# Kernel optimization log

Measured on AMD Instinct MI355X. Metric: run time of the kernel, lower is better.

The kernel has to match this reference:

```python
import jax, jax.numpy as jnp
import numpy as np

D, FF, R, B, S, H, HD = 1024, 4096, 16, 8, 512, 16, 64
EPS = 1e-5


def _lora(x, w, b, la, lb):
    # base linear (w is [out,in] torch-style) + low-rank LoRA add
    return x @ w.T + b + (x @ la) @ lb


def _ln(x, w, b):
    mu = jnp.mean(x, axis=-1, keepdims=True)
    var = jnp.mean((x - mu) ** 2, axis=-1, keepdims=True)
    return (x - mu) * jax.lax.rsqrt(var + EPS) * w + b


def setup_inputs() -> dict:
    key = jax.random.key(0)
    ks = jax.random.split(key, 32)
    i = iter(range(32))
    nrm = lambda shape, scale=0.02: jax.random.normal(ks[next(i)], shape, jnp.float32) * scale
    inp = {
        'x': jax.random.normal(ks[next(i)], (B, S, D), jnp.float32),
        'attention_mask': jnp.zeros((B, 1, 1, S), jnp.float32),
        'w_q': nrm((D, D)), 'b_q': nrm((D,)), 'la_q': nrm((D, R)), 'lb_q': nrm((R, D)),
        'w_k': nrm((D, D)), 'b_k': nrm((D,)), 'la_k': nrm((D, R)), 'lb_k': nrm((R, D)),
        'w_v': nrm((D, D)), 'b_v': nrm((D,)), 'la_v': nrm((D, R)), 'lb_v': nrm((R, D)),
        'w_o': nrm((D, D)), 'b_o': nrm((D,)), 'la_o': nrm((D, R)), 'lb_o': nrm((R, D)),
        'nw1': jnp.ones((D,), jnp.float32), 'nb1': jnp.zeros((D,), jnp.float32),
        'w_up': nrm((FF, D)), 'b_up': nrm((FF,)), 'la_up': nrm((D, R)), 'lb_up': nrm((R, FF)),
        'w_down': nrm((D, FF)), 'b_down': nrm((D,)), 'la_down': nrm((FF, R)), 'lb_down': nrm((R, D)),
        'nw2': jnp.ones((D,), jnp.float32), 'nb2': jnp.zeros((D,), jnp.float32),
        'num_heads': H, 'head_dim': HD,
    }
    return inp


def reference(x, attention_mask, w_q, b_q, la_q, lb_q, w_k, b_k, la_k, lb_k,
              w_v, b_v, la_v, lb_v, w_o, b_o, la_o, lb_o, nw1, nb1,
              w_up, b_up, la_up, lb_up, w_down, b_down, la_down, lb_down,
              nw2, nb2, num_heads, head_dim):
    bsz, q_len, d = x.shape
    to_heads = lambda t: t.reshape(bsz, q_len, num_heads, head_dim).transpose(0, 2, 1, 3)
    q = to_heads(_lora(x, w_q, b_q, la_q, lb_q))  # [B,H,S,HD]
    k = to_heads(_lora(x, w_k, b_k, la_k, lb_k))
    v = to_heads(_lora(x, w_v, b_v, la_v, lb_v))
    s = jnp.einsum('bhqd,bhkd->bhqk', q, k) / np.sqrt(head_dim) + attention_mask
    a = jax.nn.softmax(s, axis=-1)
    o = jnp.einsum('bhqk,bhkd->bhqd', a, v).transpose(0, 2, 1, 3).reshape(bsz, q_len, d)
    o_final = _lora(o, w_o, b_o, la_o, lb_o) + x
    x_medium = _ln(o_final, nw1, nb1)
    up = _lora(x_medium, w_up, b_up, la_up, lb_up)
    fn = jax.nn.gelu(up, approximate=False)  # torch F.gelu default = exact erf
    down = _lora(fn, w_down, b_down, la_down, lb_down) + x_medium
    return _ln(down, nw2, nb2)
```

## Files before the change

### kernel.cpp

```cpp
#include <hip/hip_runtime.h>
#include <math.h>

typedef unsigned short u16;
typedef __attribute__((ext_vector_type(8))) short short8;
typedef __attribute__((ext_vector_type(4))) float floatx4;

#define DEV __device__ __forceinline__

DEV u16 f2bs(float f){ union{float f; unsigned u;} v; v.f=f; unsigned r = v.u + 0x7fffu + ((v.u>>16)&1u); return (u16)(r>>16); }
DEV float bs2f(u16 u){ union{float f; unsigned u;} v; v.u = ((unsigned)u)<<16; return v.f; }

DEV float gelu_f(float x){
  float u2 = 2.f * x * (0.7978845608028654f + 0.03567740813636141f*x*x);
  float e = __expf(u2);
  float th = 1.f - 2.f/(e + 1.f);
  return 0.5f*x*(1.f + th);
}

#define GLL16(G,L) __builtin_amdgcn_global_load_lds((__attribute__((address_space(1))) const void*)(G), (__attribute__((address_space(3))) void*)(L), 16, 0, 0)

enum { EP_BF16=0, EP_F32RES=3, EP_GELU=4 };

DEV void swizzle_bid(int orig, int gx, int gy, int& bx, int& by){
  const int nwg = gx*gy;
  const int q = nwg >> 3, r = nwg & 7;
  const int xcd = orig & 7, idx = orig >> 3;
  const int logical = (xcd < r) ? xcd*(q+1) + idx : r*(q+1) + (xcd-r)*q + idx;
  const int G = 8;
  const int per = G*gx;
  const int gid = logical / per;
  const int rem = logical - gid*per;
  const int by0 = gid*G;
  const int rows = min(G, gy - by0);
  by = by0 + rem % rows;
  bx = rem / rows;
}

template<int MODE,bool LORA,bool SWZ>
__global__ __launch_bounds__(512) void gemm8(
    const u16* __restrict__ A, int lda,
    const u16* __restrict__ B, int ldb,
    int K,
    u16* __restrict__ obf, float* __restrict__ of32, int ldc,
    const float* __restrict__ bias,
    const u16* __restrict__ tA, int tlda,
    const u16* __restrict__ lbB,
    const float* __restrict__ resid)
{
  __shared__ u16 sm8[65536];
  const int tid = threadIdx.x;
  const int lane = tid & 63, wave = tid >> 6;
  const int wr = wave >> 2, wc = wave & 3;
  const int row16 = lane & 15, kgrp = lane >> 4;
  int bx = blockIdx.x, by = blockIdx.y;
  if constexpr (SWZ)
    swizzle_bid(blockIdx.y*gridDim.x + blockIdx.x, gridDim.x, gridDim.y, bx, by);
  const int bm0 = by*256, bn0 = bx*256;
  const u16* Ab = A + (long)bm0*lda;
  const u16* Bb = B + (long)bn0*ldb;
  const int tsel = (LORA && tlda==192) ? ((bn0>>10)*64) : 0;
  const int srow = lane >> 3;
  const int gcol = ((lane&7) ^ srow) * 8;
  const int nKT = K >> 6;
  const int nIT = nKT + (LORA ? 1 : 0);

  auto stage_half = [&](int kt, int h, int buf){
    const int isB = h & 1, hi = h >> 1;
    const u16* src; long ld;
    if (!LORA || kt < nKT){
      if (isB){ src = Bb + kt*64; ld = ldb; } else { src = Ab + kt*64; ld = lda; }
    } else {
      if (isB){ src = lbB + (long)bn0*64; ld = 64; }
      else    { src = tA + (long)bm0*tlda + tsel; ld = tlda; }
    }
    char* base = (char*)sm8 + buf*65536 + isB*32768 + hi*16384;
    #pragma unroll
    for (int rr=0; rr<2; ++rr){
      int g = wave + rr*8;
      GLL16(src + (long)(hi*128 + g*8 + srow)*ld + gcol, base + g*1024);
    }
  };
  auto ldA = [&](int buf, int mh, int i, int ks)->short8{
    int r_ = mh*128 + wr*64 + i*16 + row16;
    return *(const short8*)((const char*)sm8 + buf*65536 + r_*128 + (((ks*4+kgrp) ^ (r_&7))<<4));
  };
  auto ldB = [&](int buf, int nh, int j, int ks)->short8{
    int r_ = nh*128 + wc*32 + j*16 + row16;
    return *(const short8*)((const char*)sm8 + buf*65536 + 32768 + r_*128 + (((ks*4+kgrp) ^ (r_&7))<<4));
  };

  floatx4 acc[8][4];
  #pragma unroll
  for (int i=0;i<8;i++)
    #pragma unroll
    for (int j=0;j<4;j++)
      acc[i][j] = (floatx4){0.f,0.f,0.f,0.f};

  stage_half(0,0,0); stage_half(0,1,0); stage_half(0,2,0); stage_half(0,3,0);
  if (nIT>1){ stage_half(1,0,1); stage_half(1,1,1); }

#define MM8(mh,nh) \
  { _Pragma("unroll") \
    for (int i=0;i<4;i++) \
      _Pragma("unroll") \
      for (int j=0;j<2;j++) \
        _Pragma("unroll") \
        for (int ks=0;ks<2;ks++) \
          acc[(mh)*4+i][(nh)*2+j] = __builtin_amdgcn_mfma_f32_16x16x32_bf16(afr[i][ks], bfr[j][ks], acc[(mh)*4+i][(nh)*2+j], 0, 0, 0); }

  int buf = 0;
  for (int t=0; t<nIT; ++t, buf^=1){
    const bool n1 = (t+1 < nIT), n2 = (t+2 < nIT);
    short8 afr[4][2], bfr[2][2];
    if (n1) asm volatile("s_waitcnt vmcnt(4)" ::: "memory");
    else    asm volatile("s_waitcnt vmcnt(0)" ::: "memory");
    __builtin_amdgcn_s_barrier();
    #pragma unroll
    for (int i=0;i<4;i++){ afr[i][0]=ldA(buf,0,i,0); afr[i][1]=ldA(buf,0,i,1); }
    #pragma unroll
    for (int j=0;j<2;j++){ bfr[j][0]=ldB(buf,0,j,0); bfr[j][1]=ldB(buf,0,j,1); }
    if (n1){ stage_half(t+1,2,buf^1); stage_half(t+1,3,buf^1); }
    asm volatile("s_waitcnt lgkmcnt(0)" ::: "memory");
    __builtin_amdgcn_sched_barrier(0);
    __builtin_amdgcn_s_setprio(1);
    MM8(0,0);
    __builtin_amdgcn_s_setprio(0);
    __builtin_amdgcn_s_barrier();
    #pragma unroll
    for (int j=0;j<2;j++){ bfr[j][0]=ldB(buf,1,j,0); bfr[j][1]=ldB(buf,1,j,1); }
    asm volatile("s_waitcnt lgkmcnt(0)" ::: "memory");
    __builtin_amdgcn_sched_barrier(0);
    __builtin_amdgcn_s_setprio(1);
    MM8(0,1);
    __builtin_amdgcn_s_setprio(0);
    __builtin_amdgcn_s_barrier();
    #pragma unroll
    for (int i=0;i<4;i++){ afr[i][0]=ldA(buf,1,i,0); afr[i][1]=ldA(buf,1,i,1); }
    #pragma unroll
    for (int j=0;j<2;j++){ bfr[j][0]=ldB(buf,0,j,0); bfr[j][1]=ldB(buf,0,j,1); }
    if (n2) stage_half(t+2,0,buf);
    asm volatile("s_waitcnt lgkmcnt(0)" ::: "memory");
    __builtin_amdgcn_sched_barrier(0);
    __builtin_amdgcn_s_setprio(1);
    MM8(1,0);
    __builtin_amdgcn_s_setprio(0);
    __builtin_amdgcn_s_barrier();
    #pragma unroll
    for (int j=0;j<2;j++){ bfr[j][0]=ldB(buf,1,j,0); bfr[j][1]=ldB(buf,1,j,1); }
    if (n2) stage_half(t+2,1,buf);
    asm volatile("s_waitcnt lgkmcnt(0)" ::: "memory");
    __builtin_amdgcn_sched_barrier(0);
    __builtin_amdgcn_s_setprio(1);
    MM8(1,1);
    __builtin_amdgcn_s_setprio(0);
  }
#undef MM8

  #pragma unroll
  for (int mi=0;mi<8;mi++){
    const int mloc = (mi<4) ? (wr*64 + mi*16) : (128 + wr*64 + (mi-4)*16);
    #pragma unroll
    for (int r=0;r<4;r++){
      const long mg = bm0 + mloc + kgrp*4 + r;
      #pragma unroll
      for (int ni=0;ni<4;ni++){
        const int nloc = (ni<2) ? (wc*32 + ni*16) : (128 + wc*32 + (ni-2)*16);
        const int ng = bn0 + nloc + row16;
        float v = acc[mi][ni][r] + bias[ng];
        if constexpr (MODE==EP_F32RES){
          v += resid[mg*ldc + ng];
          of32[mg*ldc + ng] = v;
        } else if constexpr (MODE==EP_GELU){
          obf[mg*ldc + ng] = f2bs(gelu_f(v));
        } else {
          obf[mg*ldc + ng] = f2bs(v);
        }
      }
    }
  }
}

template<int BM,int BN,int WM,int WN,int MODE,bool LORA,bool SWZ>
__global__ __launch_bounds__((BM/WM)*(BN/WN)*64) void gemm_bt(
    const u16* __restrict__ A, int lda,
    const u16* __restrict__ B, int ldb,
    int K,
    u16* __restrict__ obf, float* __restrict__ of32, int ldc,
    const float* __restrict__ bias,
    const u16* __restrict__ tA, int tlda,
    const u16* __restrict__ lbB,
    const float* __restrict__ resid)
{
  constexpr int NWM = BM/WM, NWN = BN/WN, NW = NWM*NWN;
  constexpr int FM = WM/16, FN = WN/16;
  constexpr int TILE = (BM+BN)*64;
  constexpr int LPT = (BM+BN)/(8*NW);
  static_assert(NW==4 || NW==8, "4 or 8 waves");
  static_assert((BM/8)%NW==0 && (BN/8)%NW==0, "row-group striping");
  __shared__ u16 ab[2*TILE];

  const int tid = threadIdx.x;
  const int lane = tid & 63, wave = tid >> 6;
  const int wr = wave / NWN, wc = wave % NWN;
  const int row16 = lane & 15, kgrp = lane >> 4;
  int bx = blockIdx.x, by = blockIdx.y;
  if constexpr (SWZ)
    swizzle_bid(blockIdx.y*gridDim.x + blockIdx.x, gridDim.x, gridDim.y, bx, by);
  const int bm0 = by * BM, bn0 = bx * BN;

  const u16* Ab = A + (long)bm0*lda;
  const u16* Bb = B + (long)bn0*ldb;
  const int tsel = (LORA && tlda==192) ? ((bn0>>10)*64) : 0;
  const int srow = lane >> 3;
  const int gcol = ((lane&7) ^ srow) * 8;

  const int nKT = K >> 6;
  const int nIT = nKT + (LORA ? 1 : 0);

  auto stage = [&](int kt, int buf){
    const u16 *Ak, *Bk; long la_, lb_;
    if (!LORA || kt < nKT){ Ak = Ab + kt*64; la_ = lda; Bk = Bb + kt*64; lb_ = ldb; }
    else { Ak = tA + (long)bm0*tlda + tsel; la_ = tlda; Bk = lbB + (long)bn0*64; lb_ = 64; }
    char* l = (char*)(ab + buf*TILE);
    #pragma unroll
    for (int g0=0; g0<BM/8; g0+=NW){
      int g = g0 + wave;
      GLL16(Ak + (long)(g*8 + srow)*la_ + gcol, l + g*1024);
    }
    #pragma unroll
    for (int g0=0; g0<BN/8; g0+=NW){
      int g = g0 + wave;
      GLL16(Bk + (long)(g*8 + srow)*lb_ + gcol, l + BM*128 + g*1024);
    }
  };

  floatx4 acc[FM][FN];
  #pragma unroll
  for (int i=0;i<FM;i++)
    #pragma unroll
    for (int j=0;j<FN;j++)
      acc[i][j] = (floatx4){0.f,0.f,0.f,0.f};

  stage(0, 0);
  if (nIT > 1) stage(1, 1);
  int cur = 0;
  for (int kt=0; kt<nIT; ++kt){
    if (kt+1 < nIT) asm volatile("s_waitcnt vmcnt(%0)" :: "n"(LPT) : "memory");
    else            asm volatile("s_waitcnt vmcnt(0)" ::: "memory");
    __builtin_amdgcn_s_barrier();

    const char* lds = (const char*)(ab + cur*TILE);
    __builtin_amdgcn_s_setprio(1);
    #pragma unroll
    for (int ks=0; ks<2; ++ks){
      short8 af[FM], bfr[FN];
      #pragma unroll
      for (int mi=0;mi<FM;mi++){
        int r_ = wr*WM + mi*16 + row16;
        af[mi] = *(const short8*)(lds + r_*128 + (((ks*4 + kgrp) ^ (r_&7))<<4));
      }
      #pragma unroll
      for (int ni=0;ni<FN;ni++){
        int r_ = wc*WN + ni*16 + row16;
        bfr[ni] = *(const short8*)(lds + BM*128 + r_*128 + (((ks*4 + kgrp) ^ (r_&7))<<4));
      }
      #pragma unroll
      for (int mi=0;mi<FM;mi++)
        #pragma unroll
        for (int ni=0;ni<FN;ni++)
          acc[mi][ni] = __builtin_amdgcn_mfma_f32_16x16x32_bf16(af[mi], bfr[ni], acc[mi][ni], 0, 0, 0);
    }
    __builtin_amdgcn_s_setprio(0);

    asm volatile("s_waitcnt lgkmcnt(0)" ::: "memory");
    __builtin_amdgcn_sched_barrier(0);
    __builtin_amdgcn_s_barrier();
    if (kt+2 < nIT) stage(kt+2, cur);
    cur ^= 1;
  }

  #pragma unroll
  for (int mi=0;mi<FM;mi++){
    #pragma unroll
    for (int r=0;r<4;r++){
      const int ml = wr*WM + mi*16 + kgrp*4 + r;
      const long mg = bm0 + ml;
      #pragma unroll
      for (int ni=0;ni<FN;ni++){
        const int nl = wc*WN + ni*16 + row16;
        const int ng = bn0 + nl;
        float v = acc[mi][ni][r] + bias[ng];
        if constexpr (MODE==EP_F32RES){
          v += resid[mg*ldc + ng];
          of32[mg*ldc + ng] = v;
        } else if constexpr (MODE==EP_GELU){
          obf[mg*ldc + ng] = f2bs(gelu_f(v));
        } else {
          obf[mg*ldc + ng] = f2bs(v);
        }
      }
    }
  }
}

template<int NT>
__global__ __launch_bounds__(64) void lora_mfma(
    const u16* __restrict__ A, const int K,
    const u16* __restrict__ lat,
    u16* __restrict__ t, int tld)
{
  const int lane = threadIdx.x & 63;
  const int c = lane & 15, kg = lane >> 4;
  const int m0 = blockIdx.x * 16;
  const u16* Arow = A + (long)(m0 + c)*K + kg*8;
  const u16* Brow = lat + (long)c*K + kg*8;
  floatx4 acc[NT];
  #pragma unroll
  for (int tj=0;tj<NT;tj++) acc[tj] = (floatx4){0.f,0.f,0.f,0.f};
  const int nKS = K >> 5;
  #pragma unroll 4
  for (int ks=0; ks<nKS; ++ks){
    short8 a = *(const short8*)(Arow + ks*32);
    #pragma unroll
    for (int tj=0; tj<NT; ++tj){
      short8 b = *(const short8*)(Brow + (long)tj*16*K + ks*32);
      acc[tj] = __builtin_amdgcn_mfma_f32_16x16x32_bf16(a, b, acc[tj], 0, 0, 0);
    }
  }
  #pragma unroll
  for (int tj=0; tj<NT; ++tj)
    #pragma unroll
    for (int r=0;r<4;r++){
      u16* dst = t + (long)(m0 + kg*4 + r)*tld + tj*64;
      dst[c] = f2bs(acc[tj][r]);
      dst[16+c] = 0; dst[32+c] = 0; dst[48+c] = 0;
    }
}

__global__ __launch_bounds__(256) void flash_attn(
    const u16* __restrict__ qkv,
    const u16* __restrict__ vt,
    const float* __restrict__ mask,
    u16* __restrict__ attn_o)
{
  __shared__ u16 sm[33792];
  u16* Qs = sm;
  u16* Ps = sm + 24576;

  const int tid = threadIdx.x, lane = tid & 63, wave = tid >> 6;
  const int c = lane & 15, kg = lane >> 4;
  const int qt = blockIdx.x;
  const int z  = blockIdx.y;
  const int b = z >> 4, h = z & 15;
  const int q0 = qt * 128;
  const int srow = lane >> 3;
  const int scol = ((lane&7) ^ srow) * 8;

  const u16* kbase = qkv + ((long)(b*512))*3072 + 1024 + h*64;
  const u16* vbase = vt + (long)z*64*512;

  auto stage_kv = [&](int kv, int buf){
    char* Kd = (char*)(sm + 8192  + buf*4096);
    char* Vd = (char*)(sm + 16384 + buf*4096);
    #pragma unroll
    for (int i=0;i<2;i++){
      int rb = i*32 + wave*8;
      GLL16(kbase + (long)(kv*64 + rb + srow)*3072 + scol, Kd + rb*128);
      GLL16(vbase + (long)(rb + srow)*512 + kv*64 + scol, Vd + rb*128);
    }
  };

  {
    const u16* src = qkv + ((long)(b*512 + q0))*3072 + h*64;
    #pragma unroll
    for (int i=0;i<4;i++){
      int rb = i*32 + wave*8;
      GLL16(src + (long)(rb + srow)*3072 + scol, (char*)Qs + rb*128);
    }
  }
  stage_kv(0, 0);
  __syncthreads();

  auto ld_swz = [&](const u16* t, int row, int koff8) -> short8 {
    return *(const short8*)((const char*)t + row*128 + ((koff8 ^ (row&7))<<4));
  };

  short8 af[2][2];
  #pragma unroll
  for (int mi=0;mi<2;mi++)
    #pragma unroll
    for (int ks=0;ks<2;ks++)
      af[mi][ks] = ld_swz(Qs, wave*32 + mi*16 + c, ks*4 + kg);

  floatx4 o_acc[2][4];
  float m_run[2][4], l_run[2][4];
  #pragma unroll
  for (int mi=0;mi<2;mi++){
    #pragma unroll
    for (int dj=0;dj<4;dj++) o_acc[mi][dj] = (floatx4){0.f,0.f,0.f,0.f};
    #pragma unroll
    for (int r=0;r<4;r++){ m_run[mi][r] = -3.0e38f; l_run[mi][r] = 0.f; }
  }

  int cur = 0;
  for (int kv=0; kv<8; ++kv){
    if (kv+1 < 8) stage_kv(kv+1, cur^1);
    const u16* Ks = sm + 8192  + cur*4096;
    const u16* Vs = sm + 16384 + cur*4096;

    floatx4 s_acc[2][4];
    #pragma unroll
    for (int mi=0;mi<2;mi++)
      #pragma unroll
      for (int ni=0;ni<4;ni++)
        s_acc[mi][ni] = (floatx4){0.f,0.f,0.f,0.f};
    #pragma unroll
    for (int ks=0;ks<2;ks++){
      short8 bf[4];
      #pragma unroll
      for (int ni=0;ni<4;ni++)
        bf[ni] = ld_swz(Ks, ni*16 + c, ks*4 + kg);
      #pragma unroll
      for (int mi=0;mi<2;mi++)
        #pragma unroll
        for (int ni=0;ni<4;ni++)
          s_acc[mi][ni] = __builtin_amdgcn_mfma_f32_16x16x32_bf16(af[mi][ks], bf[ni], s_acc[mi][ni], 0, 0, 0);
    }

    float mv[4];
    #pragma unroll
    for (int ni=0;ni<4;ni++) mv[ni] = mask[b*512 + kv*64 + ni*16 + c];

    #pragma unroll
    for (int mi=0;mi<2;mi++){
      #pragma unroll
      for (int r=0;r<4;r++){
        float s0 = s_acc[mi][0][r]*0.125f + mv[0];
        float s1 = s_acc[mi][1][r]*0.125f + mv[1];
        float s2 = s_acc[mi][2][r]*0.125f + mv[2];
        float s3 = s_acc[mi][3][r]*0.125f + mv[3];
        float tmax = fmaxf(fmaxf(s0,s1), fmaxf(s2,s3));
        #pragma unroll
        for (int o=1;o<16;o<<=1) tmax = fmaxf(tmax, __shfl_xor(tmax, o));
        const float mnew = fmaxf(m_run[mi][r], tmax);
        const float p0 = __expf(s0 - mnew), p1 = __expf(s1 - mnew);
        const float p2 = __expf(s2 - mnew), p3 = __expf(s3 - mnew);
        float psum = p0+p1+p2+p3;
        #pragma unroll
        for (int o=1;o<16;o<<=1) psum += __shfl_xor(psum, o);
        const float alpha = __expf(m_run[mi][r] - mnew);
        l_run[mi][r] = l_run[mi][r]*alpha + psum;
        m_run[mi][r] = mnew;
        #pragma unroll
        for (int dj=0;dj<4;dj++) o_acc[mi][dj][r] *= alpha;
        const int rl = mi*16 + kg*4 + r;
        u16* pw = Ps + wave*2304 + rl*72;
        pw[c]      = f2bs(p0);
        pw[16 + c] = f2bs(p1);
        pw[32 + c] = f2bs(p2);
        pw[48 + c] = f2bs(p3);
      }
    }
    __syncthreads();

    #pragma unroll
    for (int ks=0;ks<2;ks++){
      short8 pa[2], vb[4];
      #pragma unroll
      for (int mi=0;mi<2;mi++)
        pa[mi] = *(const short8*)&Ps[wave*2304 + (mi*16 + c)*72 + ks*32 + kg*8];
      #pragma unroll
      for (int dj=0;dj<4;dj++)
        vb[dj] = ld_swz(Vs, dj*16 + c, ks*4 + kg);
      __builtin_amdgcn_s_setprio(1);
      #pragma unroll
      for (int mi=0;mi<2;mi++)
        #pragma unroll
        for (int dj=0;dj<4;dj++)
          o_acc[mi][dj] = __builtin_amdgcn_mfma_f32_16x16x32_bf16(pa[mi], vb[dj], o_acc[mi][dj], 0, 0, 0);
      __builtin_amdgcn_s_setprio(0);
    }
    __syncthreads();
    cur ^= 1;
  }

  #pragma unroll
  for (int mi=0;mi<2;mi++){
    #pragma unroll
    for (int r=0;r<4;r++){
      const float inv = 1.f / l_run[mi][r];
      const int s_g = q0 + wave*32 + mi*16 + kg*4 + r;
      u16* dst = attn_o + (long)(b*512 + s_g)*1024 + h*64;
      #pragma unroll
      for (int dj=0;dj<4;dj++)
        dst[dj*16 + c] = f2bs(o_acc[mi][dj][r]*inv);
    }
  }
}

__global__ __launch_bounds__(256) void convert_bulk(
  const float* __restrict__ x,
  const float* __restrict__ wq, const float* __restrict__ wk, const float* __restrict__ wv,
  const float* __restrict__ wo, const float* __restrict__ wup, const float* __restrict__ wdn,
  u16* __restrict__ xb, u16* __restrict__ wqkv, u16* __restrict__ wob,
  u16* __restrict__ wupb, u16* __restrict__ wdnb)
{
  const long NX = 4194304, NWt = 1048576;
  const long T4 = (NX + 3*NWt + NWt + NX + NX) >> 2;
  for (long i4 = (long)blockIdx.x*256 + threadIdx.x; i4 < T4; i4 += (long)gridDim.x*256){
    long j = i4 << 2;
    const float* src; u16* dst; long soff, doff;
    if (j < NX){ src=x; dst=xb; soff=j; doff=j; }
    else { j -= NX;
      if (j < 3*NWt){ int p=(int)(j>>20); src = p==0?wq:(p==1?wk:wv); dst=wqkv; soff = j & (NWt-1); doff = j; }
      else { j -= 3*NWt;
        if (j < NWt){ src=wo; dst=wob; soff=j; doff=j; }
        else { j -= NWt;
          if (j < NX){ src=wup; dst=wupb; soff=j; doff=j; }
          else { j -= NX; src=wdn; dst=wdnb; soff=j; doff=j; }
        }
      }
    }
    const float4 v = *(const float4*)(src + soff);
    ushort4 o;
    o.x = f2bs(v.x); o.y = f2bs(v.y); o.z = f2bs(v.z); o.w = f2bs(v.w);
    *(ushort4*)(dst + doff) = o;
  }
}

__global__ __launch_bounds__(256) void convert_small(
  const float* __restrict__ bq, const float* __restrict__ bk, const float* __restrict__ bv,
  const float* __restrict__ lbq, const float* __restrict__ lbk, const float* __restrict__ lbv,
  const float* __restrict__ lbo, const float* __restrict__ lbup, const float* __restrict__ lbdn,
  const float* __restrict__ laq, const float* __restrict__ lak, const float* __restrict__ lav,
  const float* __restrict__ lao, const float* __restrict__ laup, const float* __restrict__ ladn,
  float* __restrict__ biascat, u16* __restrict__ lbtqkv, u16* __restrict__ lbto,
  u16* __restrict__ lbtup, u16* __restrict__ lbtdn,
  u16* __restrict__ latqkv, u16* __restrict__ lato,
  u16* __restrict__ latup, u16* __restrict__ latdn)
{
  long i = (long)blockIdx.x*256 + threadIdx.x;
  if (i < 3072){ int p=(int)(i>>10); biascat[i] = (p==0?bq:(p==1?bk:bv))[i&1023]; return; }
  i -= 3072;
  if (i < 49152){ int k=(int)(i/3072), n=(int)(i%3072); int p=n>>10;
    const float* l = p==0?lbq:(p==1?lbk:lbv);
    u16* d = lbtqkv + (long)n*64 + k;
    d[0] = f2bs(l[k*1024 + (n&1023)]); d[16]=0; d[32]=0; d[48]=0; return; }
  i -= 49152;
  if (i < 16384){ int k=(int)(i>>10), n=(int)(i&1023);
    u16* d = lbto + (long)n*64 + k;
    d[0] = f2bs(lbo[k*1024+n]); d[16]=0; d[32]=0; d[48]=0; return; }
  i -= 16384;
  if (i < 65536){ int k=(int)(i>>12), n=(int)(i&4095);
    u16* d = lbtup + (long)n*64 + k;
    d[0] = f2bs(lbup[k*4096+n]); d[16]=0; d[32]=0; d[48]=0; return; }
  i -= 65536;
  if (i < 16384){ int k=(int)(i>>10), n=(int)(i&1023);
    u16* d = lbtdn + (long)n*64 + k;
    d[0] = f2bs(lbdn[k*1024+n]); d[16]=0; d[32]=0; d[48]=0; return; }
  i -= 16384;
  if (i < 49152){ int r=(int)(i>>10), k=(int)(i&1023);
    const float* l = r<16 ? laq : (r<32 ? lak : lav);
    latqkv[i] = f2bs(l[k*16 + (r&15)]); return; }
  i -= 49152;
  if (i < 16384){ int r=(int)(i>>10), k=(int)(i&1023);
    lato[i] = f2bs(lao[k*16+r]); return; }
  i -= 16384;
  if (i < 16384){ int r=(int)(i>>10), k=(int)(i&1023);
    latup[i] = f2bs(laup[k*16+r]); return; }
  i -= 16384;
  if (i < 65536){ int r=(int)(i>>12), k=(int)(i&4095);
    latdn[i] = f2bs(ladn[k*16+r]); }
}

__global__ __launch_bounds__(256) void transpose_v(const u16* __restrict__ qkv, u16* __restrict__ vt){
  const int st = blockIdx.x;
  const int z = blockIdx.y;
  const int b = z >> 4, h = z & 15;
  __shared__ u16 tile[64][68];
  const int t = threadIdx.x;
  const int q16 = t & 15, g16 = t >> 4;
  const u16* src = qkv + ((long)(b*512 + st*64))*3072 + 2048 + h*64;
  #pragma unroll
  for (int i=0;i<4;i++){
    int s_l = i*16 + g16;
    const u16* pp = src + (long)s_l*3072 + q16*4;
    #pragma unroll
    for (int jj=0;jj<4;jj++) tile[s_l][q16*4+jj] = pp[jj];
  }
  __syncthreads();
  u16* dst = vt + (long)z*64*512 + st*64;
  #pragma unroll
  for (int i=0;i<4;i++){
    int d_l = i*16 + g16;
    int s_l = q16*4;
    unsigned long long v = (unsigned long long)tile[s_l][d_l]
      | ((unsigned long long)tile[s_l+1][d_l] << 16)
      | ((unsigned long long)tile[s_l+2][d_l] << 32)
      | ((unsigned long long)tile[s_l+3][d_l] << 48);
    *(unsigned long long*)(dst + (long)d_l*512 + s_l) = v;
  }
}

__global__ __launch_bounds__(256) void ln_k(
    const float* __restrict__ in, float* __restrict__ outf, u16* __restrict__ outb,
    const float* __restrict__ gam, const float* __restrict__ bet)
{
  const long row = blockIdx.x;
  const float4 v = ((const float4*)(in + row*1024))[threadIdx.x];
  float s = v.x+v.y+v.z+v.w;
  float q = v.x*v.x + v.y*v.y + v.z*v.z + v.w*v.w;
  const int lane = threadIdx.x & 63, w = threadIdx.x >> 6;
  __shared__ float rs[4], rq[4];
  #pragma unroll
  for (int o=32;o;o>>=1){ s += __shfl_down(s,o); q += __shfl_down(q,o); }
  if (!lane){ rs[w]=s; rq[w]=q; }
  __syncthreads();
  const float S = rs[0]+rs[1]+rs[2]+rs[3];
  const float Q = rq[0]+rq[1]+rq[2]+rq[3];
  const float mu = S*(1.f/1024.f);
  const float var = Q*(1.f/1024.f) - mu*mu;
  const float rstd = rsqrtf(var + 1e-5f);
  const float4 g = ((const float4*)gam)[threadIdx.x];
  const float4 b = ((const float4*)bet)[threadIdx.x];
  float4 o;
  o.x = (v.x-mu)*rstd*g.x + b.x;
  o.y = (v.y-mu)*rstd*g.y + b.y;
  o.z = (v.z-mu)*rstd*g.z + b.z;
  o.w = (v.w-mu)*rstd*g.w + b.w;
  if (outf) ((float4*)(outf + row*1024))[threadIdx.x] = o;
  if (outb){
    uint2 u;
    u.x = (unsigned)f2bs(o.x) | ((unsigned)f2bs(o.y) << 16);
    u.y = (unsigned)f2bs(o.z) | ((unsigned)f2bs(o.w) << 16);
    ((uint2*)(outb + row*1024))[threadIdx.x] = u;
  }
}

extern "C" void kernel_launch(void* const* d_in, const int* in_sizes, int n_in,
                              void* d_out, int out_size, void* d_ws, size_t ws_size,
                              hipStream_t stream) {
  const float* x      = (const float*)d_in[0];
  const float* mask   = (const float*)d_in[1];
  const float* w_q    = (const float*)d_in[2];
  const float* b_q    = (const float*)d_in[3];
  const float* la_q   = (const float*)d_in[4];
  const float* lb_q   = (const float*)d_in[5];
  const float* w_k    = (const float*)d_in[6];
  const float* b_k    = (const float*)d_in[7];
  const float* la_k   = (const float*)d_in[8];
  const float* lb_k   = (const float*)d_in[9];
  const float* w_v    = (const float*)d_in[10];
  const float* b_v    = (const float*)d_in[11];
  const float* la_v   = (const float*)d_in[12];
  const float* lb_v   = (const float*)d_in[13];
  const float* w_o    = (const float*)d_in[14];
  const float* b_o    = (const float*)d_in[15];
  const float* la_o   = (const float*)d_in[16];
  const float* lb_o   = (const float*)d_in[17];
  const float* nw1    = (const float*)d_in[18];
  const float* nb1    = (const float*)d_in[19];
  const float* w_up   = (const float*)d_in[20];
  const float* b_up   = (const float*)d_in[21];
  const float* la_up  = (const float*)d_in[22];
  const float* lb_up  = (const float*)d_in[23];
  const float* w_dn   = (const float*)d_in[24];
  const float* b_dn   = (const float*)d_in[25];
  const float* la_dn  = (const float*)d_in[26];
  const float* lb_dn  = (const float*)d_in[27];
  const float* nw2    = (const float*)d_in[28];
  const float* nb2    = (const float*)d_in[29];
  float* out = (float*)d_out;

  char* ws = (char*)d_ws;
  size_t used = 0;
  auto alloc = [&](size_t bytes) -> char* {
    char* p = ws + used;
    used += (bytes + 255) & ~(size_t)255;
    return p;
  };
  u16*   xb      = (u16*)  alloc(4194304*2);
  u16*   wqkv    = (u16*)  alloc(3145728*2);
  u16*   wob     = (u16*)  alloc(1048576*2);
  u16*   wupb    = (u16*)  alloc(4194304*2);
  u16*   wdnb    = (u16*)  alloc(4194304*2);
  float* biascat = (float*)alloc(3072*4);
  u16*   lbtqkv  = (u16*)  alloc((size_t)3072*64*2);
  u16*   lbto    = (u16*)  alloc((size_t)1024*64*2);
  u16*   lbtup   = (u16*)  alloc((size_t)4096*64*2);
  u16*   lbtdn   = (u16*)  alloc((size_t)1024*64*2);
  u16*   latqkv  = (u16*)  alloc(48*1024*2);
  u16*   lato    = (u16*)  alloc(16*1024*2);
  u16*   latup   = (u16*)  alloc(16*1024*2);
  u16*   latdn   = (u16*)  alloc(16*4096*2);
  u16*   t_all   = (u16*)  alloc((size_t)4096*192*2);
  u16*   t_o     = (u16*)  alloc((size_t)4096*64*2);
  u16*   t_up    = (u16*)  alloc((size_t)4096*64*2);
  u16*   t_dn    = (u16*)  alloc((size_t)4096*64*2);
  u16*   qkv     = (u16*)  alloc((size_t)4096*3072*2);
  u16*   vt      = (u16*)  alloc((size_t)128*64*512*2);
  u16*   attn_o  = (u16*)  alloc(4194304*2);
  float* o_final = (float*)alloc((size_t)4194304*4);
  float* x_med   = (float*)alloc((size_t)4194304*4);
  u16*   x_med_b = (u16*)  alloc(4194304*2);
  u16*   fn      = (u16*)  alloc((size_t)4096*4096*2);
  if (used > ws_size) return;

  convert_bulk<<<2048, 256, 0, stream>>>(x, w_q, w_k, w_v, w_o, w_up, w_dn,
                                         xb, wqkv, wob, wupb, wdnb);
  convert_small<<<1164, 256, 0, stream>>>(b_q, b_k, b_v, lb_q, lb_k, lb_v,
                                          lb_o, lb_up, lb_dn,
                                          la_q, la_k, la_v, la_o, la_up, la_dn,
                                          biascat, lbtqkv, lbto, lbtup, lbtdn,
                                          latqkv, lato, latup, latdn);
  lora_mfma<3><<<256, 64, 0, stream>>>(xb, 1024, latqkv, t_all, 192);
  gemm8<EP_BF16,true,true><<<dim3(12,16,1), 512, 0, stream>>>(
      xb, 1024, wqkv, 1024, 1024, qkv, nullptr, 3072,
      biascat, t_all, 192, lbtqkv, nullptr);
  transpose_v<<<dim3(8,128), 256, 0, stream>>>(qkv, vt);
  flash_attn<<<dim3(4,128), 256, 0, stream>>>(qkv, vt, mask, attn_o);
  lora_mfma<1><<<256, 64, 0, stream>>>(attn_o, 1024, lato, t_o, 64);
  gemm_bt<64,128,32,64,EP_F32RES,true,true><<<dim3(8,64,1), 256, 0, stream>>>(
      attn_o, 1024, wob, 1024, 1024, nullptr, o_final, 1024,
      b_o, t_o, 64, lbto, x);
  ln_k<<<4096, 256, 0, stream>>>(o_final, x_med, x_med_b, nw1, nb1);
  lora_mfma<1><<<256, 64, 0, stream>>>(x_med_b, 1024, latup, t_up, 64);
  gemm8<EP_GELU,true,true><<<dim3(16,16,1), 512, 0, stream>>>(
      x_med_b, 1024, wupb, 1024, 1024, fn, nullptr, 4096,
      b_up, t_up, 64, lbtup, nullptr);
  lora_mfma<1><<<256, 64, 0, stream>>>(fn, 4096, latdn, t_dn, 64);
  gemm_bt<64,128,32,64,EP_F32RES,true,true><<<dim3(8,64,1), 256, 0, stream>>>(
      fn, 4096, wdnb, 4096, 4096, nullptr, out, 1024,
      b_dn, t_dn, 64, lbtdn, x_med);
  ln_k<<<4096, 256, 0, stream>>>(out, out, nullptr, nw2, nb2);
}
```

Measured before the change: 276.1 us.

## Restructure GEMM main loop to load all fragments once and cut barriers

Each K-iteration of the 256x256 GEMM now loads the A and B fragments for both halves once into separate registers (a0,a1,b0,b1). Before, B fragments were reloaded from LDS across four sub-phases. The next-tile stage is issued at the top of the loop, partial lgkmcnt waits overlap LDS reads with MFMA, and only two barriers remain per iteration instead of four. Launch bounds request 2 blocks per CU. Register pressure rises, and with __launch_bounds__(512,2) this may cause spills or lower occupancy. The earlier issue of global-to-LDS loads also changes the vmcnt accounting, which risks correctness if the wait counts are wrong.

```diff
diff --git a/kernel.cpp b/kernel.cpp
--- a/kernel.cpp
+++ b/kernel.cpp
@@ -18,6 +18,7 @@
 }
 
 #define GLL16(G,L) __builtin_amdgcn_global_load_lds((__attribute__((address_space(1))) const void*)(G), (__attribute__((address_space(3))) void*)(L), 16, 0, 0)
+#define SB0() __builtin_amdgcn_sched_barrier(0)
 
 enum { EP_BF16=0, EP_F32RES=3, EP_GELU=4 };
 
@@ -37,7 +38,7 @@
 }
 
 template<int MODE,bool LORA,bool SWZ>
-__global__ __launch_bounds__(512) void gemm8(
+__global__ __launch_bounds__(512,2) void gemm8(
     const u16* __restrict__ A, int lda,
     const u16* __restrict__ B, int ldb,
     int K,
@@ -99,59 +100,51 @@
   stage_half(0,0,0); stage_half(0,1,0); stage_half(0,2,0); stage_half(0,3,0);
   if (nIT>1){ stage_half(1,0,1); stage_half(1,1,1); }
 
-#define MM8(mh,nh) \
+#define MM8(mh,nh,AR,BR) \
   { _Pragma("unroll") \
     for (int i=0;i<4;i++) \
       _Pragma("unroll") \
       for (int j=0;j<2;j++) \
         _Pragma("unroll") \
         for (int ks=0;ks<2;ks++) \
-          acc[(mh)*4+i][(nh)*2+j] = __builtin_amdgcn_mfma_f32_16x16x32_bf16(afr[i][ks], bfr[j][ks], acc[(mh)*4+i][(nh)*2+j], 0, 0, 0); }
+          acc[(mh)*4+i][(nh)*2+j] = __builtin_amdgcn_mfma_f32_16x16x32_bf16(AR[i][ks], BR[j][ks], acc[(mh)*4+i][(nh)*2+j], 0, 0, 0); }
 
   int buf = 0;
   for (int t=0; t<nIT; ++t, buf^=1){
     const bool n1 = (t+1 < nIT), n2 = (t+2 < nIT);
-    short8 afr[4][2], bfr[2][2];
-    if (n1) asm volatile("s_waitcnt vmcnt(4)" ::: "memory");
+    if (n1){ stage_half(t+1,2,buf^1); stage_half(t+1,3,buf^1); }
+    if (n1) asm volatile("s_waitcnt vmcnt(8)" ::: "memory");
     else    asm volatile("s_waitcnt vmcnt(0)" ::: "memory");
     __builtin_amdgcn_s_barrier();
-    #pragma unroll
-    for (int i=0;i<4;i++){ afr[i][0]=ldA(buf,0,i,0); afr[i][1]=ldA(buf,0,i,1); }
-    #pragma unroll
-    for (int j=0;j<2;j++){ bfr[j][0]=ldB(buf,0,j,0); bfr[j][1]=ldB(buf,0,j,1); }
-    if (n1){ stage_half(t+1,2,buf^1); stage_half(t+1,3,buf^1); }
+
+    short8 a0[4][2], a1[4][2], b0[2][2], b1[2][2];
+    #pragma unroll
+    for (int i=0;i<4;i++){ a0[i][0]=ldA(buf,0,i,0); a0[i][1]=ldA(buf,0,i,1); }
+    #pragma unroll
+    for (int j=0;j<2;j++){ b0[j][0]=ldB(buf,0,j,0); b0[j][1]=ldB(buf,0,j,1); }
+    SB0();
+    #pragma unroll
+    for (int j=0;j<2;j++){ b1[j][0]=ldB(buf,1,j,0); b1[j][1]=ldB(buf,1,j,1); }
+    asm volatile("s_waitcnt lgkmcnt(4)" ::: "memory");
+    SB0();
+    __builtin_amdgcn_s_setprio(1);
+    MM8(0,0,a0,b0);
+    __builtin_amdgcn_s_setprio(0);
+    SB0();
+    #pragma unroll
+    for (int i=0;i<4;i++){ a1[i][0]=ldA(buf,1,i,0); a1[i][1]=ldA(buf,1,i,1); }
+    asm volatile("s_waitcnt lgkmcnt(8)" ::: "memory");
+    SB0();
+    __builtin_amdgcn_s_setprio(1);
+    MM8(0,1,a0,b1);
+    __builtin_amdgcn_s_setprio(0);
     asm volatile("s_waitcnt lgkmcnt(0)" ::: "memory");
-    __builtin_amdgcn_sched_barrier(0);
+    SB0();
+    __builtin_amdgcn_s_barrier();
+    if (n2){ stage_half(t+2,0,buf); stage_half(t+2,1,buf); }
     __builtin_amdgcn_s_setprio(1);
-    MM8(0,0);
-    __builtin_amdgcn_s_setprio(0);
-    __builtin_amdgcn_s_barrier();
-    #pragma unroll
-    for (int j=0;j<2;j++){ bfr[j][0]=ldB(buf,1,j,0); bfr[j][1]=ldB(buf,1,j,1); }
-    asm volatile("s_waitcnt lgkmcnt(0)" ::: "memory");
-    __builtin_amdgcn_sched_barrier(0);
-    __builtin_amdgcn_s_setprio(1);
-    MM8(0,1);
-    __builtin_amdgcn_s_setprio(0);
-    __builtin_amdgcn_s_barrier();
-    #pragma unroll
-    for (int i=0;i<4;i++){ afr[i][0]=ldA(buf,1,i,0); afr[i][1]=ldA(buf,1,i,1); }
-    #pragma unroll
-    for (int j=0;j<2;j++){ bfr[j][0]=ldB(buf,0,j,0); bfr[j][1]=ldB(buf,0,j,1); }
-    if (n2) stage_half(t+2,0,buf);
-    asm volatile("s_waitcnt lgkmcnt(0)" ::: "memory");
-    __builtin_amdgcn_sched_barrier(0);
-    __builtin_amdgcn_s_setprio(1);
-    MM8(1,0);
-    __builtin_amdgcn_s_setprio(0);
-    __builtin_amdgcn_s_barrier();
-    #pragma unroll
-    for (int j=0;j<2;j++){ bfr[j][0]=ldB(buf,1,j,0); bfr[j][1]=ldB(buf,1,j,1); }
-    if (n2) stage_half(t+2,1,buf);
-    asm volatile("s_waitcnt lgkmcnt(0)" ::: "memory");
-    __builtin_amdgcn_sched_barrier(0);
-    __builtin_amdgcn_s_setprio(1);
-    MM8(1,1);
+    MM8(1,1,a1,b1);
+    MM8(1,0,a1,b0);
     __builtin_amdgcn_s_setprio(0);
   }
 #undef MM8
```

Result: no change. 274.7 us (-0.5%).
